# Kernel tuning notes

Hardware: AMD Instinct MI355X
Metric: run time of the kernel (lower is better)

The kernel has to match this reference:

```python
import jax, jax.numpy as jnp
import numpy as np

EMB = 1024
HEADS = 16
HEAD_DIM = EMB // HEADS
DIM_FF = 4096
EPS = 1e-05


def layer_norm(x, gain, bias):
    # BasicLayerNorm: (x - mean) / (std + eps), std with unbiased=False
    mean = jnp.mean(x, axis=-1, keepdims=True)
    std = jnp.sqrt(jnp.mean((x - mean) ** 2, axis=-1, keepdims=True))
    return gain * ((x - mean) / (std + EPS)) + bias


def setup_inputs() -> dict:
    key = jax.random.key(0)
    ks = jax.random.split(key, 8)
    scale = 1.0 / np.sqrt(EMB)
    x = jax.random.normal(ks[0], (4, 2048, EMB), dtype=jnp.float32)
    Wq = jax.random.normal(ks[1], (EMB, EMB), dtype=jnp.float32) * scale
    Wk = jax.random.normal(ks[2], (EMB, EMB), dtype=jnp.float32) * scale
    Wv = jax.random.normal(ks[3], (EMB, EMB), dtype=jnp.float32) * scale
    Wo = jax.random.normal(ks[4], (EMB, EMB), dtype=jnp.float32) * scale
    W1 = jax.random.normal(ks[5], (EMB, DIM_FF), dtype=jnp.float32) * scale
    b1 = jnp.zeros((DIM_FF,), dtype=jnp.float32)
    W2 = jax.random.normal(ks[6], (DIM_FF, EMB), dtype=jnp.float32) * (1.0 / np.sqrt(DIM_FF))
    b2 = jnp.zeros((EMB,), dtype=jnp.float32)
    gain1 = jnp.ones((EMB,), dtype=jnp.float32)
    bias1 = jnp.zeros((EMB,), dtype=jnp.float32)
    gain2 = jnp.ones((EMB,), dtype=jnp.float32)
    bias2 = jnp.zeros((EMB,), dtype=jnp.float32)
    return dict(x=x, Wq=Wq, Wk=Wk, Wv=Wv, Wo=Wo, W1=W1, b1=b1, W2=W2, b2=b2,
                gain1=gain1, bias1=bias1, gain2=gain2, bias2=bias2)


def reference(x, Wq, Wk, Wv, Wo, W1, b1, W2, b2, gain1, bias1, gain2, bias2):
    b, t, e = x.shape
    h, dk = HEADS, HEAD_DIM
    # QKV projections, split heads -> (b, h, t, dk)
    q = (x @ Wq).reshape(b, t, h, dk).transpose(0, 2, 1, 3)
    k = (x @ Wk).reshape(b, t, h, dk).transpose(0, 2, 1, 3)
    v = (x @ Wv).reshape(b, t, h, dk).transpose(0, 2, 1, 3)
    # scaled dot-product attention
    scores = jnp.einsum('bhqd,bhkd->bhqk', q, k) / jnp.sqrt(jnp.float32(dk))
    attn = jax.nn.softmax(scores, axis=-1)
    ctx = jnp.einsum('bhqk,bhkd->bhqd', attn, v)
    # merge heads and output projection
    merged = ctx.transpose(0, 2, 1, 3).reshape(b, t, e)
    attended = merged @ Wo
    # residual + layer norm 1 (dropout is identity at inference)
    x1 = layer_norm(attended + x, gain1, bias1)
    # feed-forward
    ff = jax.nn.relu(x1 @ W1 + b1) @ W2 + b2
    # residual + layer norm 2
    return layer_norm(ff + x1, gain2, bias2)
```

## Files before the change

kernel.cpp:

```cpp
#include <hip/hip_runtime.h>
#include <hip/hip_bf16.h>
#include <math.h>

#define EMB 1024
#define DIM_FF 4096
#define HEADS 16
#define HD 64
#define TSEQ 2048
#define BATCH 4
#define MROWS (BATCH*TSEQ)
#define LN_EPS 1e-5f
#define QSCALE 0.18033688011f

typedef __attribute__((ext_vector_type(8))) short short8;
typedef __attribute__((ext_vector_type(4))) float f32x4;
typedef __attribute__((ext_vector_type(16))) float f32x16;

#define MFMA16(a,b,c) __builtin_amdgcn_mfma_f32_16x16x32_bf16((a),(b),(c),0,0,0)
#define MFMA32(a,b,c) __builtin_amdgcn_mfma_f32_32x32x16_bf16((a),(b),(c),0,0,0)

#define GLOBAL_AS(p) ((const __attribute__((address_space(1))) void*)(p))
#define LDS_AS(p)    ((__attribute__((address_space(3))) void*)(p))

__device__ __forceinline__ unsigned cvtpk_bf16(float lo, float hi){
    unsigned r;
    asm("v_cvt_pk_bf16_f32 %0, %1, %2" : "=v"(r) : "v"(lo), "v"(hi));
    return r;
}
__device__ __forceinline__ f32x4 ld4bf(const __hip_bfloat16* p){
    ushort4 u = *reinterpret_cast<const ushort4*>(p);
    union{unsigned i; float f;} c0,c1,c2,c3;
    c0.i=(unsigned)u.x<<16; c1.i=(unsigned)u.y<<16; c2.i=(unsigned)u.z<<16; c3.i=(unsigned)u.w<<16;
    f32x4 r; r[0]=c0.f; r[1]=c1.f; r[2]=c2.f; r[3]=c3.f;
    return r;
}

__global__ __launch_bounds__(256)
void cvt_bf16(const float* __restrict__ in, __hip_bfloat16* __restrict__ out, int n4){
    int i = blockIdx.x*256 + threadIdx.x;
    if (i >= n4) return;
    f32x4 v = reinterpret_cast<const f32x4*>(in)[i];
    uint2 o;
    o.x = cvtpk_bf16(v[0], v[1]);
    o.y = cvtpk_bf16(v[2], v[3]);
    *reinterpret_cast<uint2*>(reinterpret_cast<unsigned short*>(out) + (size_t)i*4) = o;
}

__global__ __launch_bounds__(256)
void transpose_cvt4(const float* __restrict__ s0, const float* __restrict__ s1,
                    const float* __restrict__ s2, const float* __restrict__ s3,
                    __hip_bfloat16* __restrict__ out){
    const float* in = blockIdx.z==0 ? s0 : blockIdx.z==1 ? s1 : blockIdx.z==2 ? s2 : s3;
    __hip_bfloat16* dst = out + (size_t)blockIdx.z*1024*1024;
    __shared__ __hip_bfloat16 tile[32][33];
    int bx = blockIdx.x*32, by = blockIdx.y*32;
    int x = bx + threadIdx.x;
    #pragma unroll
    for (int i = threadIdx.y; i < 32; i += 8)
        tile[i][threadIdx.x] = __float2bfloat16(in[(size_t)(by+i)*1024 + x]);
    __syncthreads();
    int xo = by + threadIdx.x;
    #pragma unroll
    for (int i = threadIdx.y; i < 32; i += 8)
        dst[(size_t)(bx+i)*1024 + xo] = tile[threadIdx.x][i];
}

__global__ __launch_bounds__(256)
void transpose_cvt(const float* __restrict__ in, __hip_bfloat16* __restrict__ out, int R, int C){
    __shared__ __hip_bfloat16 tile[32][33];
    int bx = blockIdx.x*32, by = blockIdx.y*32;
    int x = bx + threadIdx.x;
    #pragma unroll
    for (int i = threadIdx.y; i < 32; i += 8)
        tile[i][threadIdx.x] = __float2bfloat16(in[(size_t)(by+i)*C + x]);
    __syncthreads();
    int xo = by + threadIdx.x;
    #pragma unroll
    for (int i = threadIdx.y; i < 32; i += 8)
        out[(size_t)(bx+i)*R + xo] = tile[threadIdx.x][i];
}

template<int EPI>
__global__ __launch_bounds__(256, 2)
void gemm_bt(const __hip_bfloat16* __restrict__ A,
             const __hip_bfloat16* __restrict__ Bt,
             int M, int N, int K,
             __hip_bfloat16* __restrict__ Cb,
             const float* __restrict__ bias)
{
    __shared__ __align__(16) __hip_bfloat16 As[128*32];
    __shared__ __align__(16) __hip_bfloat16 Bs[128*32];
    const int tid = threadIdx.x;
    const int lane = tid & 63;
    const int wid = tid >> 6;
    const int wm = wid >> 1, wn = wid & 1;
    const int row0 = blockIdx.x * 128;
    const int col0 = blockIdx.y * 128;
    const int rA = lane & 15, kg = lane >> 4;

    const int lrow = lane >> 2;
    const int lcol = (lane & 3) << 3;

    f32x4 acc[4][4] = {};

    for (int kt = 0; kt < K; kt += 32) {
        __syncthreads();
        #pragma unroll
        for (int half = 0; half < 2; ++half) {
            const int rbase = (wid << 5) + (half << 4);
            const int r = rbase + lrow;
            __builtin_amdgcn_global_load_lds(
                GLOBAL_AS(A + (size_t)(row0 + r)*K + kt + lcol),
                LDS_AS(&As[rbase*32]), 16, 0, 0);
            __builtin_amdgcn_global_load_lds(
                GLOBAL_AS(Bt + (size_t)(col0 + r)*K + kt + lcol),
                LDS_AS(&Bs[rbase*32]), 16, 0, 0);
        }
        __syncthreads();
        short8 af[4], bfr[4];
        #pragma unroll
        for (int mi = 0; mi < 4; ++mi)
            af[mi] = *reinterpret_cast<const short8*>(&As[(wm*64 + mi*16 + rA)*32 + (kg<<3)]);
        #pragma unroll
        for (int ni = 0; ni < 4; ++ni)
            bfr[ni] = *reinterpret_cast<const short8*>(&Bs[(wn*64 + ni*16 + rA)*32 + (kg<<3)]);
        #pragma unroll
        for (int mi = 0; mi < 4; ++mi)
            #pragma unroll
            for (int ni = 0; ni < 4; ++ni)
                acc[mi][ni] = MFMA16(af[mi], bfr[ni], acc[mi][ni]);
    }

    #pragma unroll
    for (int mi=0; mi<4; ++mi) {
        #pragma unroll
        for (int ni=0; ni<4; ++ni) {
            #pragma unroll
            for (int j=0;j<4;++j){
                float v = acc[mi][ni][j];
                int grow = row0 + wm*64 + mi*16 + (kg<<2) + j;
                int gcol = col0 + wn*64 + ni*16 + rA;
                if constexpr (EPI==3) v += bias[gcol];
                Cb[(size_t)grow*N + gcol] = __float2bfloat16(v);
            }
        }
    }
}

#define GPHASE(P, STAGE_EXPR, WAIT_EXPR) do { \
    short8 af[2][2]; \
    _Pragma("unroll") \
    for (int i_=0;i_<2;++i_){ \
      _Pragma("unroll") \
      for (int kk_=0;kk_<2;++kk_) \
        af[i_][kk_] = *reinterpret_cast<const short8*>(pA + ((2*(P)+i_)*16+rA)*128 + (((kk_<<2)+kg)^swz)*16); \
    } \
    STAGE_EXPR; WAIT_EXPR; \
    __builtin_amdgcn_s_barrier(); \
    __builtin_amdgcn_s_setprio(1); \
    _Pragma("unroll") \
    for (int i_=0;i_<2;++i_){ \
      _Pragma("unroll") \
      for (int ni_=0;ni_<4;++ni_){ \
        acc[2*(P)+i_][ni_] = MFMA16(af[i_][0], bfr[ni_][0], acc[2*(P)+i_][ni_]); \
        acc[2*(P)+i_][ni_] = MFMA16(af[i_][1], bfr[ni_][1], acc[2*(P)+i_][ni_]); \
      } \
    } \
    __builtin_amdgcn_s_setprio(0); \
    __builtin_amdgcn_s_barrier(); \
} while(0)

template<int EPI>
__global__ __launch_bounds__(512, 2)
void gemm256(const __hip_bfloat16* __restrict__ A,
             const __hip_bfloat16* __restrict__ Bt,
             int M, int N, int K,
             __hip_bfloat16* __restrict__ Cb,
             const float* __restrict__ bias,
             __hip_bfloat16* __restrict__ qo,
             __hip_bfloat16* __restrict__ ko,
             __hip_bfloat16* __restrict__ vto)
{
    __shared__ __align__(16) __hip_bfloat16 Al[2][16384];
    __shared__ __align__(16) __hip_bfloat16 Bl[2][16384];
    const int tid = threadIdx.x;
    const int lane = tid & 63;
    const int wid = tid >> 6;
    const int wm = wid >> 2, wn = wid & 3;
    const int row0 = blockIdx.x * 256;
    const int col0 = blockIdx.y * 256;
    const int rA = lane & 15, kg = lane >> 4, swz = rA & 7;
    const int NT = K >> 6;

    const int lr = lane >> 3;
    const int lg = (lane & 7) ^ lr;
    const __hip_bfloat16* sA = A  + (size_t)(row0 + wid*8 + lr)*K + lg*8;
    const __hip_bfloat16* sB = Bt + (size_t)(col0 + wid*8 + lr)*K + lg*8;
    char* dA = (char*)&Al[0][0] + wid*8*128;
    char* dB = (char*)&Bl[0][0] + wid*8*128;

    auto stage = [&](const __hip_bfloat16* s, char* d, int buf, int half, int kt){
        #pragma unroll
        for (int rr = 0; rr < 2; ++rr)
            __builtin_amdgcn_global_load_lds(
                GLOBAL_AS(s + (size_t)(half*128 + rr*64)*K + kt),
                LDS_AS(d + buf*32768 + (half*128 + rr*64)*128), 16, 0, 0);
    };

    f32x4 acc[8][4] = {};

    stage(sA, dA, 0, 0, 0); stage(sA, dA, 0, 1, 0);
    stage(sB, dB, 0, 0, 0); stage(sB, dB, 0, 1, 0);
    stage(sB, dB, 1, 0, 64); stage(sB, dB, 1, 1, 64);
    asm volatile("s_waitcnt vmcnt(4)" ::: "memory");
    __builtin_amdgcn_sched_barrier(0);
    __builtin_amdgcn_s_barrier();

    const char* cA = (const char*)&Al[0][0] + wm*128*128;
    const char* cB = (const char*)&Bl[0][0] + wn*64*128;

    for (int t = 0; t < NT; ++t) {
        const int buf = t & 1;
        const char* pA = cA + buf*32768;
        const char* pB = cB + buf*32768;
        short8 bfr[4][2];
        #pragma unroll
        for (int ni = 0; ni < 4; ++ni)
            #pragma unroll
            for (int kk = 0; kk < 2; ++kk)
                bfr[ni][kk] = *reinterpret_cast<const short8*>(pB + (ni*16+rA)*128 + (((kk<<2)+kg)^swz)*16);

        GPHASE(0, if (t+1 < NT) stage(sA, dA, buf^1, 0, (t+1)*64), );
        GPHASE(1, if (t+1 < NT) stage(sA, dA, buf^1, 1, (t+1)*64), );
        GPHASE(2, if (t+2 < NT) stage(sB, dB, buf,   0, (t+2)*64), );
        GPHASE(3, if (t+2 < NT) stage(sB, dB, buf,   1, (t+2)*64),
            if (t+2 < NT) { asm volatile("s_waitcnt vmcnt(4)" ::: "memory"); }
            else          { asm volatile("s_waitcnt vmcnt(0)" ::: "memory"); }
            __builtin_amdgcn_sched_barrier(0) );
    }

    #pragma unroll
    for (int mi=0; mi<8; ++mi) {
        #pragma unroll
        for (int ni=0; ni<4; ++ni) {
            #pragma unroll
            for (int j=0;j<4;++j){
                float v = acc[mi][ni][j];
                int grow = row0 + wm*128 + mi*16 + (kg<<2) + j;
                int gcol = col0 + wn*64 + ni*16 + rA;
                if constexpr (EPI==0) {
                    int b = grow >> 11, t = grow & 2047;
                    int which = gcol >> 10, hdx = gcol & 1023;
                    int h = hdx >> 6, d = hdx & 63;
                    int bh = b*HEADS + h;
                    if (which==0)      qo[((size_t)bh*TSEQ + t)*HD + d] = __float2bfloat16(v*QSCALE);
                    else if (which==1) ko[((size_t)bh*TSEQ + t)*HD + d] = __float2bfloat16(v);
                    else               vto[((size_t)bh*HD + d)*TSEQ + t] = __float2bfloat16(v);
                } else {
                    v += bias[gcol]; v = v > 0.0f ? v : 0.0f;
                    Cb[(size_t)grow*N + gcol] = __float2bfloat16(v);
                }
            }
        }
    }
}

__global__ __launch_bounds__(256, 4)
void attn_fwd(const __hip_bfloat16* __restrict__ q,
              const __hip_bfloat16* __restrict__ k,
              const __hip_bfloat16* __restrict__ vt,
              __hip_bfloat16* __restrict__ merged)
{
    const int wg = (blockIdx.x & 7) * 128 + (blockIdx.x >> 3);
    const int bh = wg >> 4;
    const int qt = wg & 15;
    const int wid = threadIdx.x >> 6, lane = threadIdx.x & 63;
    const int l31 = lane & 31;
    const int hi  = lane >> 5;
    const int swz = lane & 7;
    const int qrow0 = qt*128 + wid*32;
    const __hip_bfloat16* Qh = q  + (size_t)bh*TSEQ*HD;
    const __hip_bfloat16* Kh = k  + (size_t)bh*TSEQ*HD;
    const __hip_bfloat16* Vh = vt + (size_t)bh*HD*TSEQ;

    __shared__ __align__(16) __hip_bfloat16 Kl[2][64*64];
    __shared__ __align__(16) __hip_bfloat16 Vl[2][64*64];

    short8 qv[4];
    #pragma unroll
    for (int c=0;c<4;++c)
        qv[c] = *reinterpret_cast<const short8*>(Qh + (size_t)(qrow0+l31)*HD + c*16 + hi*8);

    const int lrow = lane >> 3;
    const int lslot = ((lane & 7) ^ lrow) << 3;
    const __hip_bfloat16* sK0 = Kh + (size_t)(wid*16 + lrow)*HD + lslot;
    const __hip_bfloat16* sV0 = Vh + (size_t)(wid*16 + lrow)*TSEQ + lslot;
    const int dOff = wid*16*64;

    f32x16 O0 = {}, O1 = {};
    float lpart = 0.f;
    short8 paf[4] = {};

    __builtin_amdgcn_global_load_lds(GLOBAL_AS(sK0),        LDS_AS(&Kl[0][dOff]),        16, 0, 0);
    __builtin_amdgcn_global_load_lds(GLOBAL_AS(sK0 + 8*HD), LDS_AS(&Kl[0][dOff + 8*64]), 16, 0, 0);
    __syncthreads();

    const int NT = TSEQ/64;
    for (int t = 0; t < NT; ++t) {
        const int b = t & 1;
        if (t+1 < NT) {
            const int kt = (t+1)*64;
            __builtin_amdgcn_global_load_lds(GLOBAL_AS(sK0 + (size_t)kt*HD),     LDS_AS(&Kl[b^1][dOff]),        16, 0, 0);
            __builtin_amdgcn_global_load_lds(GLOBAL_AS(sK0 + (size_t)(kt+8)*HD), LDS_AS(&Kl[b^1][dOff + 8*64]), 16, 0, 0);
        }
        __builtin_amdgcn_global_load_lds(GLOBAL_AS(sV0 + t*64),          LDS_AS(&Vl[b][dOff]),        16, 0, 0);
        __builtin_amdgcn_global_load_lds(GLOBAL_AS(sV0 + 8*TSEQ + t*64), LDS_AS(&Vl[b][dOff + 8*64]), 16, 0, 0);

        const char* Kb  = (const char*)&Kl[b][0];
        const char* Vbp = (const char*)&Vl[b^1][0];

        f32x16 st0 = {}, st1 = {};
        #pragma unroll
        for (int c=0;c<4;++c) {
            short8 ka0 = *reinterpret_cast<const short8*>(Kb + l31*128      + (((2*c+hi)^swz)<<4));
            short8 ka1 = *reinterpret_cast<const short8*>(Kb + (32+l31)*128 + (((2*c+hi)^swz)<<4));
            st0 = MFMA32(ka0, qv[c], st0);
            st1 = MFMA32(ka1, qv[c], st1);
        }

        if (t > 0) {
            #pragma unroll
            for (int kc=0; kc<4; ++kc) {
                short8 vf0 = *reinterpret_cast<const short8*>(Vbp + l31*128      + (((2*kc+hi)^swz)<<4));
                short8 vf1 = *reinterpret_cast<const short8*>(Vbp + (32+l31)*128 + (((2*kc+hi)^swz)<<4));
                O0 = MFMA32(paf[kc], vf0, O0);
                O1 = MFMA32(paf[kc], vf1, O1);
            }
        }

        #pragma unroll
        for (int r=0;r<16;++r) {
            st0[r] = __builtin_amdgcn_exp2f(st0[r]);
            st1[r] = __builtin_amdgcn_exp2f(st1[r]);
        }
        {
            f32x16 ss = st0 + st1;
            float s8 = (((ss[0]+ss[1])+(ss[2]+ss[3]))+((ss[4]+ss[5])+(ss[6]+ss[7])))
                     + (((ss[8]+ss[9])+(ss[10]+ss[11]))+((ss[12]+ss[13])+(ss[14]+ss[15])));
            lpart += s8;
        }
        unsigned pk0[8], pk1[8];
        #pragma unroll
        for (int j=0;j<8;++j) {
            pk0[j] = cvtpk_bf16(st0[2*j], st0[2*j+1]);
            pk1[j] = cvtpk_bf16(st1[2*j], st1[2*j+1]);
        }
        #pragma unroll
        for (int kc=0; kc<4; ++kc) {
            const unsigned* pkt = (kc>>1) ? pk1 : pk0;
            const int j0 = 4*(kc&1);
            unsigned swA = (unsigned)__shfl_xor((int)pkt[j0+0], 32);
            unsigned swB = (unsigned)__shfl_xor((int)pkt[j0+1], 32);
            unsigned swC = (unsigned)__shfl_xor((int)pkt[j0+2], 32);
            unsigned swD = (unsigned)__shfl_xor((int)pkt[j0+3], 32);
            union { unsigned u[4]; short8 s; } pa;
            pa.u[0] = hi ? swC : pkt[j0+0];
            pa.u[1] = hi ? swD : pkt[j0+1];
            pa.u[2] = hi ? pkt[j0+2] : swA;
            pa.u[3] = hi ? pkt[j0+3] : swB;
            paf[kc] = pa.s;
        }
        __syncthreads();
    }
    {
        const char* Vbp = (const char*)&Vl[(NT-1)&1][0];
        #pragma unroll
        for (int kc=0; kc<4; ++kc) {
            short8 vf0 = *reinterpret_cast<const short8*>(Vbp + l31*128      + (((2*kc+hi)^swz)<<4));
            short8 vf1 = *reinterpret_cast<const short8*>(Vbp + (32+l31)*128 + (((2*kc+hi)^swz)<<4));
            O0 = MFMA32(paf[kc], vf0, O0);
            O1 = MFMA32(paf[kc], vf1, O1);
        }
    }

    lpart += __shfl_xor(lpart, 32);
    float linv = 1.0f / lpart;
    const int b = bh >> 4, h = bh & 15;
    #pragma unroll
    for (int r=0;r<16;++r){
        int qp = (r&3) + 8*(r>>2) + 4*hi;
        float lr = __shfl(linv, qp);
        size_t base = ((size_t)(b*TSEQ + qrow0 + qp))*EMB + h*HD;
        merged[base + l31]      = __float2bfloat16(O0[r]*lr);
        merged[base + 32 + l31] = __float2bfloat16(O1[r]*lr);
    }
}

template<int ABF, int RBF>
__global__ __launch_bounds__(256)
void ln_res(const void* __restrict__ a_, const void* __restrict__ res_,
            const float* __restrict__ gain, const float* __restrict__ bias,
            float* __restrict__ outf, __hip_bfloat16* __restrict__ outb)
{
    const int row = blockIdx.x;
    const int tid = threadIdx.x;
    const int lane = tid & 63, wid = tid >> 6;
    const size_t base = (size_t)row * EMB;
    f32x4 va, vr;
    if constexpr (ABF) va = ld4bf((const __hip_bfloat16*)a_ + base + tid*4);
    else               va = *reinterpret_cast<const f32x4*>((const float*)a_ + base + tid*4);
    if constexpr (RBF) vr = ld4bf((const __hip_bfloat16*)res_ + base + tid*4);
    else               vr = *reinterpret_cast<const f32x4*>((const float*)res_ + base + tid*4);
    f32x4 v = va + vr;
    float s = v[0]+v[1]+v[2]+v[3];
    #pragma unroll
    for (int off=1; off<64; off<<=1) s += __shfl_xor(s, off);
    __shared__ float red1[4], red2[4];
    if (lane==0) red1[wid] = s;
    __syncthreads();
    float mean = (red1[0]+red1[1]+red1[2]+red1[3]) * (1.0f/EMB);
    f32x4 d;
    #pragma unroll
    for (int j=0;j<4;++j) d[j] = v[j] - mean;
    float qs = d[0]*d[0]+d[1]*d[1]+d[2]*d[2]+d[3]*d[3];
    #pragma unroll
    for (int off=1; off<64; off<<=1) qs += __shfl_xor(qs, off);
    if (lane==0) red2[wid] = qs;
    __syncthreads();
    float var = (red2[0]+red2[1]+red2[2]+red2[3]) * (1.0f/EMB);
    float r = 1.0f/(sqrtf(var)+LN_EPS);
    f32x4 g = *reinterpret_cast<const f32x4*>(gain + tid*4);
    f32x4 bb = *reinterpret_cast<const f32x4*>(bias + tid*4);
    f32x4 o;
    #pragma unroll
    for (int j=0;j<4;++j) o[j] = g[j]*(d[j]*r) + bb[j];
    if (outf)
        *reinterpret_cast<f32x4*>(outf + base + tid*4) = o;
    if (outb) {
        uint2 ob;
        ob.x = cvtpk_bf16(o[0], o[1]);
        ob.y = cvtpk_bf16(o[2], o[3]);
        *reinterpret_cast<uint2*>(reinterpret_cast<unsigned short*>(outb) + base + tid*4) = ob;
    }
}

extern "C" void kernel_launch(void* const* d_in, const int* in_sizes, int n_in,
                              void* d_out, int out_size, void* d_ws, size_t ws_size,
                              hipStream_t stream) {
    const float* x   = (const float*)d_in[0];
    const float* Wq  = (const float*)d_in[1];
    const float* Wk  = (const float*)d_in[2];
    const float* Wv  = (const float*)d_in[3];
    const float* Wo  = (const float*)d_in[4];
    const float* W1  = (const float*)d_in[5];
    const float* b1  = (const float*)d_in[6];
    const float* W2  = (const float*)d_in[7];
    const float* b2  = (const float*)d_in[8];
    const float* gain1 = (const float*)d_in[9];
    const float* bias1 = (const float*)d_in[10];
    const float* gain2 = (const float*)d_in[11];
    const float* bias2 = (const float*)d_in[12];

    char* ws = (char*)d_ws;
    __hip_bfloat16* Wqkv_t   = (__hip_bfloat16*)(ws + 0);
    __hip_bfloat16* Wo_t     = (__hip_bfloat16*)(ws + 6291456);
    __hip_bfloat16* W1_t     = (__hip_bfloat16*)(ws + 8388608);
    __hip_bfloat16* W2_t     = (__hip_bfloat16*)(ws + 16777216);
    __hip_bfloat16* xb       = (__hip_bfloat16*)(ws + 25165824);
    __hip_bfloat16* qb       = (__hip_bfloat16*)(ws + 41943040);
    __hip_bfloat16* kbuf     = (__hip_bfloat16*)(ws + 58720256);
    __hip_bfloat16* vtb      = (__hip_bfloat16*)(ws + 75497472);
    __hip_bfloat16* h1       = (__hip_bfloat16*)(ws + 25165824);
    __hip_bfloat16* mergedb  = (__hip_bfloat16*)(ws + 92274688);
    __hip_bfloat16* ffb      = (__hip_bfloat16*)(ws + 92274688);
    __hip_bfloat16* attendedb= (__hip_bfloat16*)(ws + 109051904);
    __hip_bfloat16* x1b      = (__hip_bfloat16*)(ws + 125829120);
    float*          outf     = (float*)d_out;

    dim3 tb(32,8);
    transpose_cvt4<<<dim3(32,32,4), tb, 0, stream>>>(Wq, Wk, Wv, Wo, Wqkv_t);
    transpose_cvt<<<dim3(128,32), tb, 0, stream>>>(W1, W1_t, 1024, 4096);
    transpose_cvt<<<dim3(32,128), tb, 0, stream>>>(W2, W2_t, 4096, 1024);
    cvt_bf16<<<(MROWS*EMB/4 + 255)/256, 256, 0, stream>>>(x, xb, MROWS*EMB/4);

    gemm256<0><<<dim3(MROWS/256, 3072/256), 512, 0, stream>>>(
        xb, Wqkv_t, MROWS, 3072, EMB, nullptr, nullptr, qb, kbuf, vtb);
    attn_fwd<<<dim3(1024), 256, 0, stream>>>(qb, kbuf, vtb, mergedb);
    gemm_bt<1><<<dim3(MROWS/128, EMB/128), 256, 0, stream>>>(
        mergedb, Wo_t, MROWS, EMB, EMB, attendedb, nullptr);
    ln_res<1,0><<<MROWS, 256, 0, stream>>>(attendedb, x, gain1, bias1, nullptr, x1b);
    gemm256<2><<<dim3(MROWS/256, DIM_FF/256), 512, 0, stream>>>(
        x1b, W1_t, MROWS, DIM_FF, EMB, h1, b1, nullptr, nullptr, nullptr);
    gemm_bt<3><<<dim3(MROWS/128, EMB/128), 256, 0, stream>>>(
        h1, W2_t, MROWS, EMB, DIM_FF, ffb, b2);
    ln_res<1,1><<<MROWS, 256, 0, stream>>>(ffb, x1b, gain2, bias2, outf, nullptr);
}
```

Baseline: 421.2 us.

## Triple-buffer K in attention, use permlane32 swap, read bf16 residual in LN1

The attention kernel moves from double to triple buffering of K tiles, prefetching two tiles ahead. It replaces __syncthreads with an explicit vmcnt wait plus s_barrier so loads stay in flight across iterations. The P-fragment lane exchange now uses v_permlane32_swap instead of four shuffles and selects. LN1 reads the residual from the bf16 copy of x rather than fp32, which reduces memory traffic but lowers residual precision, and it depends on the template flag meaning bf16 input.

```diff
diff --git a/kernel.cpp b/kernel.cpp
--- a/kernel.cpp
+++ b/kernel.cpp
@@ -26,6 +26,9 @@
     unsigned r;
     asm("v_cvt_pk_bf16_f32 %0, %1, %2" : "=v"(r) : "v"(lo), "v"(hi));
     return r;
+}
+__device__ __forceinline__ void permswap(unsigned &a, unsigned &b){
+    asm("v_permlane32_swap_b32 %0, %1" : "+v"(a), "+v"(b));
 }
 __device__ __forceinline__ f32x4 ld4bf(const __hip_bfloat16* p){
     ushort4 u = *reinterpret_cast<const ushort4*>(p);
@@ -283,7 +286,7 @@
     const __hip_bfloat16* Kh = k  + (size_t)bh*TSEQ*HD;
     const __hip_bfloat16* Vh = vt + (size_t)bh*HD*TSEQ;
 
-    __shared__ __align__(16) __hip_bfloat16 Kl[2][64*64];
+    __shared__ __align__(16) __hip_bfloat16 Kl[3][64*64];
     __shared__ __align__(16) __hip_bfloat16 Vl[2][64*64];
 
     short8 qv[4];
@@ -301,23 +304,29 @@
     float lpart = 0.f;
     short8 paf[4] = {};
 
-    __builtin_amdgcn_global_load_lds(GLOBAL_AS(sK0),        LDS_AS(&Kl[0][dOff]),        16, 0, 0);
-    __builtin_amdgcn_global_load_lds(GLOBAL_AS(sK0 + 8*HD), LDS_AS(&Kl[0][dOff + 8*64]), 16, 0, 0);
-    __syncthreads();
+    auto stK = [&](int t){
+        const int kt = t*64;
+        __hip_bfloat16* dst = &Kl[t%3][dOff];
+        __builtin_amdgcn_global_load_lds(GLOBAL_AS(sK0 + (size_t)kt*HD),     LDS_AS(dst),        16, 0, 0);
+        __builtin_amdgcn_global_load_lds(GLOBAL_AS(sK0 + (size_t)(kt+8)*HD), LDS_AS(dst + 8*64), 16, 0, 0);
+    };
+    auto stV = [&](int t){
+        __hip_bfloat16* dst = &Vl[t&1][dOff];
+        __builtin_amdgcn_global_load_lds(GLOBAL_AS(sV0 + t*64),          LDS_AS(dst),        16, 0, 0);
+        __builtin_amdgcn_global_load_lds(GLOBAL_AS(sV0 + 8*TSEQ + t*64), LDS_AS(dst + 8*64), 16, 0, 0);
+    };
 
     const int NT = TSEQ/64;
+    stK(0); stK(1);
+    asm volatile("s_waitcnt vmcnt(2)" ::: "memory");
+    __builtin_amdgcn_s_barrier();
+
     for (int t = 0; t < NT; ++t) {
-        const int b = t & 1;
-        if (t+1 < NT) {
-            const int kt = (t+1)*64;
-            __builtin_amdgcn_global_load_lds(GLOBAL_AS(sK0 + (size_t)kt*HD),     LDS_AS(&Kl[b^1][dOff]),        16, 0, 0);
-            __builtin_amdgcn_global_load_lds(GLOBAL_AS(sK0 + (size_t)(kt+8)*HD), LDS_AS(&Kl[b^1][dOff + 8*64]), 16, 0, 0);
-        }
-        __builtin_amdgcn_global_load_lds(GLOBAL_AS(sV0 + t*64),          LDS_AS(&Vl[b][dOff]),        16, 0, 0);
-        __builtin_amdgcn_global_load_lds(GLOBAL_AS(sV0 + 8*TSEQ + t*64), LDS_AS(&Vl[b][dOff + 8*64]), 16, 0, 0);
-
-        const char* Kb  = (const char*)&Kl[b][0];
-        const char* Vbp = (const char*)&Vl[b^1][0];
+        stV(t);
+        if (t+2 < NT) stK(t+2);
+
+        const char* Kb  = (const char*)&Kl[t%3][0];
+        const char* Vbp = (const char*)&Vl[(t-1)&1][0];
 
         f32x16 st0 = {}, st1 = {};
         #pragma unroll
@@ -357,20 +366,20 @@
         }
         #pragma unroll
         for (int kc=0; kc<4; ++kc) {
-            const unsigned* pkt = (kc>>1) ? pk1 : pk0;
+            unsigned* pkt = (kc>>1) ? pk1 : pk0;
             const int j0 = 4*(kc&1);
-            unsigned swA = (unsigned)__shfl_xor((int)pkt[j0+0], 32);
-            unsigned swB = (unsigned)__shfl_xor((int)pkt[j0+1], 32);
-            unsigned swC = (unsigned)__shfl_xor((int)pkt[j0+2], 32);
-            unsigned swD = (unsigned)__shfl_xor((int)pkt[j0+3], 32);
+            unsigned a0 = pkt[j0+0], b0 = pkt[j0+2];
+            unsigned a1 = pkt[j0+1], b1 = pkt[j0+3];
+            permswap(a0, b0);
+            permswap(a1, b1);
             union { unsigned u[4]; short8 s; } pa;
-            pa.u[0] = hi ? swC : pkt[j0+0];
-            pa.u[1] = hi ? swD : pkt[j0+1];
-            pa.u[2] = hi ? pkt[j0+2] : swA;
-            pa.u[3] = hi ? pkt[j0+3] : swB;
+            pa.u[0] = a0; pa.u[1] = a1; pa.u[2] = b0; pa.u[3] = b1;
             paf[kc] = pa.s;
         }
-        __syncthreads();
+
+        if (t+2 < NT) { asm volatile("s_waitcnt vmcnt(2)" ::: "memory"); }
+        else          { asm volatile("s_waitcnt vmcnt(0)" ::: "memory"); }
+        __builtin_amdgcn_s_barrier();
     }
     {
         const char* Vbp = (const char*)&Vl[(NT-1)&1][0];
@@ -488,7 +497,7 @@
     attn_fwd<<<dim3(1024), 256, 0, stream>>>(qb, kbuf, vtb, mergedb);
     gemm_bt<1><<<dim3(MROWS/128, EMB/128), 256, 0, stream>>>(
         mergedb, Wo_t, MROWS, EMB, EMB, attendedb, nullptr);
-    ln_res<1,0><<<MROWS, 256, 0, stream>>>(attendedb, x, gain1, bias1, nullptr, x1b);
+    ln_res<1,1><<<MROWS, 256, 0, stream>>>(attendedb, xb, gain1, bias1, nullptr, x1b);
     gemm256<2><<<dim3(MROWS/256, DIM_FF/256), 512, 0, stream>>>(
         x1b, W1_t, MROWS, DIM_FF, EMB, h1, b1, nullptr, nullptr, nullptr);
     gemm_bt<3><<<dim3(MROWS/128, EMB/128), 256, 0, stream>>>(
```

After: 406.5 us. 1.04x faster.
